# Kernel tuning notes

Measured on AMD Instinct MI355X. Metric: run time of the kernel, lower is better.

## Reference

```python
import jax, jax.numpy as jnp
import numpy as np

NH = 12  # attention heads (bert-base)


def _ln(x, s, b, eps=1e-12):
    mu = x.mean(-1, keepdims=True)
    var = ((x - mu) ** 2).mean(-1, keepdims=True)
    return (x - mu) / jnp.sqrt(var + eps) * s + b


def _forward(input_ids, token_type_ids, attention_mask, word_emb, pos_emb, type_emb,
             emb_ln_s, emb_ln_b, memory, q_w, q_b, k_w, k_b, v_w, v_b, o_w, o_b,
             ln1_s, ln1_b, f_w1, f_b1, f_w2, f_b2, ln2_s, ln2_b,
             key_w1, key_b1, key_w2, key_b2, val_w1, val_b1, val_w2, val_b2):
    B, S = input_ids.shape
    M, H = memory.shape
    T = S + M
    m = attention_mask.astype(jnp.int32)          # [B,S] 0/1
    L = m.sum(-1)                                 # [B] number of real tokens
    tok_emb = word_emb[input_ids]                 # [B,S,H]
    # stable argsort puts mask==1 positions first (in original order), then mask==0
    order = jnp.argsort(1 - m, axis=-1)           # [B,S]
    p = jnp.arange(T)[None, :]                    # [1,T]
    Lb = L[:, None]
    # output layout per sample: [real tokens (L), memory (M), pad tokens (S-L)]
    src_p = jnp.clip(jnp.where(p < Lb, p, p - M), 0, S - 1)
    src_idx = jnp.take_along_axis(order, src_p, axis=1)                  # [B,T]
    gathered = jnp.take_along_axis(tok_emb, src_idx[..., None], axis=1)  # [B,T,H]
    is_mem = (p >= Lb) & (p < Lb + M)
    mem_idx = jnp.clip(p - Lb, 0, M - 1)
    emb = jnp.where(is_mem[..., None], memory[mem_idx], gathered)        # spliced embeds
    att = (p < Lb + M).astype(emb.dtype)                                 # [B,T]
    tt = jnp.where(p < Lb, jnp.take_along_axis(token_type_ids.astype(jnp.int32), src_idx, axis=1), 1)
    # --- BERT encoder on inputs_embeds ---
    x = _ln(emb + pos_emb[None, :T] + type_emb[tt], emb_ln_s, emb_ln_b)
    bias = ((1.0 - att) * -10000.0)[:, None, None, :]                    # [B,1,1,T]
    dh = H // NH
    for l in range(q_w.shape[0]):
        q = (x @ q_w[l] + q_b[l]).reshape(B, T, NH, dh)
        k = (x @ k_w[l] + k_b[l]).reshape(B, T, NH, dh)
        v = (x @ v_w[l] + v_b[l]).reshape(B, T, NH, dh)
        s = jnp.einsum('bqhd,bkhd->bhqk', q, k) / jnp.sqrt(jnp.asarray(dh, x.dtype)) + bias
        a = jax.nn.softmax(s, axis=-1)
        ctx = jnp.einsum('bhqk,bkhd->bqhd', a, v).reshape(B, T, H)
        x = _ln(x + ctx @ o_w[l] + o_b[l], ln1_s[l], ln1_b[l])
        h = jax.nn.gelu(x @ f_w1[l] + f_b1[l], approximate=False)
        x = _ln(x + h @ f_w2[l] + f_b2[l], ln2_s[l], ln2_b[l])
    # --- gated key/value softmax pooling (get_rep_no_vae) ---
    value = jnp.tanh(jax.nn.relu(x @ val_w1 + val_b1) @ val_w2 + val_b2)       # [B,T,E]
    weight = jax.nn.sigmoid(jax.nn.relu(x @ key_w1 + key_b1) @ key_w2 + key_b2)  # [B,T,E]
    pool_mask = jnp.where(tt == 1, -jnp.inf, 0.0).astype(x.dtype)[..., None]   # [B,T,1]
    fw = jax.nn.softmax(weight + pool_mask, axis=-2)  # softmax over token dim
    return jax.nn.relu((fw * value).sum(-2))          # [B,E]


def setup_inputs() -> dict:
    key = jax.random.key(0)
    ks = jax.random.split(key, 20)
    B, S, M, H, E, V, NL, FF = 8, 512, 64, 768, 512, 30522, 2, 3072
    def rn(k, shape, s=0.02):
        return jax.random.normal(k, shape, jnp.float32) * s
    return {
        'input_ids': jax.random.randint(ks[0], (B, S), 0, V),
        'token_type_ids': jnp.zeros((B, S), jnp.int32),
        'attention_mask': jax.random.randint(ks[1], (B, S), 0, 2),
        'word_emb': rn(ks[2], (V, H)),
        'pos_emb': rn(ks[3], (S + M, H)),
        'type_emb': rn(ks[4], (2, H)),
        'emb_ln_s': jnp.ones((H,), jnp.float32), 'emb_ln_b': jnp.zeros((H,), jnp.float32),
        'memory': rn(ks[5], (M, H), 1.0),
        'q_w': rn(ks[6], (NL, H, H)), 'q_b': jnp.zeros((NL, H), jnp.float32),
        'k_w': rn(ks[7], (NL, H, H)), 'k_b': jnp.zeros((NL, H), jnp.float32),
        'v_w': rn(ks[8], (NL, H, H)), 'v_b': jnp.zeros((NL, H), jnp.float32),
        'o_w': rn(ks[9], (NL, H, H)), 'o_b': jnp.zeros((NL, H), jnp.float32),
        'ln1_s': jnp.ones((NL, H), jnp.float32), 'ln1_b': jnp.zeros((NL, H), jnp.float32),
        'f_w1': rn(ks[10], (NL, H, FF)), 'f_b1': jnp.zeros((NL, FF), jnp.float32),
        'f_w2': rn(ks[11], (NL, FF, H)), 'f_b2': jnp.zeros((NL, H), jnp.float32),
        'ln2_s': jnp.ones((NL, H), jnp.float32), 'ln2_b': jnp.zeros((NL, H), jnp.float32),
        'key_w1': rn(ks[12], (H, 2 * H)), 'key_b1': jnp.zeros((2 * H,), jnp.float32),
        'key_w2': rn(ks[13], (2 * H, E)), 'key_b2': jnp.zeros((E,), jnp.float32),
        'val_w1': rn(ks[14], (H, 2 * E)), 'val_b1': jnp.zeros((2 * E,), jnp.float32),
        'val_w2': rn(ks[15], (2 * E, E)), 'val_b2': jnp.zeros((E,), jnp.float32),
    }


def reference(input_ids, token_type_ids, attention_mask, word_emb, pos_emb, type_emb,
              emb_ln_s, emb_ln_b, memory, q_w, q_b, k_w, k_b, v_w, v_b, o_w, o_b,
              ln1_s, ln1_b, f_w1, f_b1, f_w2, f_b2, ln2_s, ln2_b,
              key_w1, key_b1, key_w2, key_b2, val_w1, val_b1, val_w2, val_b2):
    return _forward(input_ids, token_type_ids, attention_mask, word_emb, pos_emb, type_emb,
                    emb_ln_s, emb_ln_b, memory, q_w, q_b, k_w, k_b, v_w, v_b, o_w, o_b,
                    ln1_s, ln1_b, f_w1, f_b1, f_w2, f_b2, ln2_s, ln2_b,
                    key_w1, key_b1, key_w2, key_b2, val_w1, val_b1, val_w2, val_b2)
```

## Files before the change

kernel.cpp:

```cpp
#include <hip/hip_runtime.h>
#include <hip/hip_bf16.h>

#define B 8
#define S 512
#define MM 64
#define T 576
#define H 768
#define NH 12
#define DH 64
#define FF 3072
#define E 512
#define NL 2

typedef __attribute__((ext_vector_type(8))) short bf16x8;
typedef __attribute__((ext_vector_type(4))) float f32x4;

__device__ inline unsigned short bf16_rne(float f) {
    unsigned u = __builtin_bit_cast(unsigned, f);
    unsigned r = u + 0x7FFFu + ((u >> 16) & 1u);
    return (unsigned short)(r >> 16);
}

__device__ inline f32x4 mfma16(bf16x8 a, bf16x8 b, f32x4 c) {
    return __builtin_amdgcn_mfma_f32_16x16x32_bf16(a, b, c, 0, 0, 0);
}

__device__ inline void load_lds16(const void* g, void* l) {
    __builtin_amdgcn_global_load_lds((const __attribute__((address_space(1))) void*)g,
                                     (__attribute__((address_space(3))) void*)l, 16, 0, 0);
}

__global__ void order_kernel(const int* __restrict__ mask, int* __restrict__ ord,
                             int* __restrict__ Larr) {
    __shared__ int ps[S];
    int b = blockIdx.x;
    int t = threadIdx.x;
    int mv = (mask[b * S + t] != 0) ? 1 : 0;
    ps[t] = mv;
    __syncthreads();
    for (int off = 1; off < S; off <<= 1) {
        int v = ps[t];
        int add = (t >= off) ? ps[t - off] : 0;
        __syncthreads();
        ps[t] = v + add;
        __syncthreads();
    }
    int L = ps[S - 1];
    int rank = mv ? (ps[t] - 1) : (L + (t - ps[t]));
    ord[b * S + rank] = t;
    if (t == 0) Larr[b] = L;
}

__global__ void embed_kernel(const int* __restrict__ ids, const int* __restrict__ toktype,
                             const int* __restrict__ ord, const int* __restrict__ Larr,
                             int* __restrict__ boff, int* __restrict__ rowb,
                             const float* __restrict__ word_emb, const float* __restrict__ pos_emb,
                             const float* __restrict__ type_emb, const float* __restrict__ memory,
                             const float* __restrict__ lns, const float* __restrict__ lnb,
                             float* __restrict__ x, unsigned short* __restrict__ xb,
                             int* __restrict__ ttarr) {
    int t = blockIdx.x;
    int b = blockIdx.y;
    int pre[B + 1];
    {
        int acc = 0;
        #pragma unroll
        for (int b2 = 0; b2 < B; ++b2) { pre[b2] = acc; acc += Larr[b2] + MM; }
        pre[B] = acc;
    }
    int Lb = Larr[b];
    int tid = threadIdx.x;
    if (t == 0 && b == 0) {
        if (tid <= B) boff[tid] = pre[tid];
        for (int r = tid; r < B * T; r += 256) {
            int bb = 0;
            #pragma unroll
            for (int b2 = 1; b2 < B; ++b2) bb += (r >= pre[b2]) ? 1 : 0;
            rowb[r] = bb;
        }
    }
    if (t >= Lb + MM) return;
    int row = pre[b] + t;
    int tt;
    const float* src;
    if (t < Lb) {
        int sp = ord[b * S + t];
        tt = toktype[b * S + sp];
        src = &word_emb[(size_t)ids[b * S + sp] * H];
    } else {
        tt = 1;
        src = &memory[(size_t)(t - Lb) * H];
    }
    __shared__ float rowv[H];
    __shared__ float r1[256], r2[256];
    float lsum = 0.f, lsq = 0.f;
    for (int hh = tid; hh < H; hh += 256) {
        float v = src[hh] + pos_emb[(size_t)t * H + hh] + type_emb[(size_t)tt * H + hh];
        rowv[hh] = v;
        lsum += v;
        lsq += v * v;
    }
    r1[tid] = lsum; r2[tid] = lsq;
    __syncthreads();
    for (int s = 128; s > 0; s >>= 1) {
        if (tid < s) { r1[tid] += r1[tid + s]; r2[tid] += r2[tid + s]; }
        __syncthreads();
    }
    float mu = r1[0] / H;
    float var = r2[0] / H - mu * mu;
    float inv = rsqrtf(var + 1e-12f);
    for (int hh = tid; hh < H; hh += 256) {
        float v = (rowv[hh] - mu) * inv * lns[hh] + lnb[hh];
        x[(size_t)row * H + hh] = v;
        xb[(size_t)row * H + hh] = bf16_rne(v);
    }
    if (tid == 0) ttarr[row] = tt;
}

#define ACT_NONE 0
#define ACT_RELU 1
#define ACT_GELU 2
#define ACT_SIGMOID 3
#define ACT_TANH 4

template <int ACT>
__device__ inline float apply_act(float v) {
    if constexpr (ACT == ACT_RELU) return fmaxf(v, 0.f);
    else if constexpr (ACT == ACT_GELU) {
        float y = v * 0.70710678118654752f;
        float a = fabsf(y);
        float t = 1.f / (1.f + 0.3275911f * a);
        float poly = t * (0.254829592f + t * (-0.284496736f + t * (1.421413741f +
                     t * (-1.453152027f + t * 1.061405429f))));
        float e = poly * exp2f(-a * a * 1.4426950408889634f);
        float erfv = 1.f - e;
        erfv = (y < 0.f) ? -erfv : erfv;
        return 0.5f * v * (1.f + erfv);
    }
    else if constexpr (ACT == ACT_SIGMOID) return 1.f / (1.f + expf(-v));
    else if constexpr (ACT == ACT_TANH) return tanhf(v);
    else return v;
}

struct TDesc { const float* src; unsigned dstoff; int Kd; int Nd; int tile0; };
struct TTab { TDesc d[16]; int n; };

__global__ __launch_bounds__(256) void transpose_all(TTab tab, unsigned short* __restrict__ dstbase) {
    int tile = blockIdx.x;
    int mi = 0;
    #pragma unroll
    for (int i = 1; i < 16; ++i)
        if (i < tab.n && tab.d[i].tile0 <= tile) mi = i;
    TDesc d = tab.d[mi];
    int rel = tile - d.tile0;
    int tilesK = d.Kd >> 5;
    int kt = rel % tilesK, nt = rel / tilesK;
    __shared__ float ts[32][33];
    int k0 = kt * 32, n0 = nt * 32;
    int tx = threadIdx.x & 31, ty = threadIdx.x >> 5;
    #pragma unroll
    for (int r = 0; r < 4; ++r) {
        int kk = ty + r * 8;
        ts[kk][tx] = d.src[(size_t)(k0 + kk) * d.Nd + n0 + tx];
    }
    __syncthreads();
    unsigned short* Wt = dstbase + d.dstoff;
    #pragma unroll
    for (int r = 0; r < 4; ++r) {
        int nn = ty + r * 8;
        Wt[(size_t)(n0 + nn) * d.Kd + k0 + tx] = bf16_rne(ts[tx][nn]);
    }
}

#define EPI_F32   0
#define EPI_BF16  1
#define EPI_QKV   2
#define EPI_SPLIT2 3

template <int ACT, int EPI, int NSPLIT>
__global__ __launch_bounds__(256) void mfma_gemm(
    const unsigned short* __restrict__ A, const unsigned short* __restrict__ Bt,
    const float* __restrict__ b0, const float* __restrict__ b1, const float* __restrict__ b2,
    int sp1, int sp2,
    float* __restrict__ Cf, float* __restrict__ Cf2,
    float* __restrict__ Cf3, float* __restrict__ Cf4,
    unsigned short* __restrict__ Cb, unsigned short* __restrict__ Cb2,
    unsigned short* __restrict__ Vt, int n2w,
    const int* __restrict__ boffs, const int* __restrict__ rowb,
    int Mdim, int Ndim, int Kdim) {
    __shared__ unsigned short As[2][128 * 32];
    __shared__ unsigned short Bs[2][128 * 32];

    const int bn = blockIdx.x * 128, bm = blockIdx.y * 128;

    const int Mtot = boffs[B];
    if (bm >= Mtot) return;

    const int z = (NSPLIT > 1) ? blockIdx.z : 0;
    const int Klocal = Kdim / NSPLIT;
    const int koff = z * Klocal;

    const int tid = threadIdx.x;
    const int w = tid >> 6, lane = tid & 63;
    const int lr = lane & 15, g = lane >> 4;
    const int wr = w >> 1, wc = w & 1;
    f32x4 acc[4][4] = {};

    const int srow = w * 32 + (lane >> 2);
    const int kc = (((lane & 3) ^ ((lane >> 4) & 3)) * 8);
    const unsigned short* ga0 = A + (size_t)(bm + srow) * Kdim + kc;
    const unsigned short* ga1 = A + (size_t)(bm + srow + 16) * Kdim + kc;
    const unsigned short* gb0 = Bt + (size_t)(bn + srow) * Kdim + kc;
    const unsigned short* gb1 = Bt + (size_t)(bn + srow + 16) * Kdim + kc;
    const int d0 = (w * 32) * 32, d1 = (w * 32 + 16) * 32;

    const int sw = ((g ^ ((lr >> 2) & 3)) & 3) * 8;

    auto stage = [&](int pp, int k0) {
        load_lds16(ga0 + k0, &As[pp][d0]);
        load_lds16(ga1 + k0, &As[pp][d1]);
        load_lds16(gb0 + k0, &Bs[pp][d0]);
        load_lds16(gb1 + k0, &Bs[pp][d1]);
    };
    auto compute = [&](int pp) {
        bf16x8 af[4], bfr[4];
        #pragma unroll
        for (int i = 0; i < 4; ++i)
            af[i] = *(const bf16x8*)&As[pp][(wr * 64 + i * 16 + lr) * 32 + sw];
        #pragma unroll
        for (int j = 0; j < 4; ++j)
            bfr[j] = *(const bf16x8*)&Bs[pp][(wc * 64 + j * 16 + lr) * 32 + sw];
        __builtin_amdgcn_s_setprio(1);
        #pragma unroll
        for (int i = 0; i < 4; ++i)
            #pragma unroll
            for (int j = 0; j < 4; ++j)
                acc[i][j] = mfma16(af[i], bfr[j], acc[i][j]);
        __builtin_amdgcn_s_setprio(0);
    };

    const int nk = Klocal >> 5;
    stage(0, koff);
    int p = 0;
    for (int s = 0; s < nk; ++s) {
        if (s + 1 < nk) {
            stage(p ^ 1, koff + (s + 1) * 32);
            asm volatile("s_waitcnt vmcnt(4)" ::: "memory");
        } else {
            asm volatile("s_waitcnt vmcnt(0)" ::: "memory");
        }
        __builtin_amdgcn_s_barrier();
        __builtin_amdgcn_sched_barrier(0);
        compute(p);
        __builtin_amdgcn_sched_barrier(0);
        __builtin_amdgcn_s_barrier();
        __builtin_amdgcn_sched_barrier(0);
        p ^= 1;
    }

    float* Cdst = (z == 0) ? Cf : (z == 1) ? Cf2 : (z == 2) ? Cf3 : Cf4;
    #pragma unroll
    for (int i = 0; i < 4; ++i) {
        const int row0 = bm + wr * 64 + i * 16 + 4 * g;
        #pragma unroll
        for (int j = 0; j < 4; ++j) {
            const int col = bn + wc * 64 + j * 16 + lr;
            float bv = (NSPLIT > 1 && z != 0) ? 0.f
                     : ((col < sp1) ? b0[col] : (col < sp2 ? b1[col - sp1] : b2[col - sp2]));
            float vv[4];
            #pragma unroll
            for (int r = 0; r < 4; ++r) vv[r] = apply_act<ACT>(acc[i][j][r] + bv);
            if constexpr (EPI == EPI_F32) {
                #pragma unroll
                for (int r = 0; r < 4; ++r) Cdst[(size_t)(row0 + r) * Ndim + col] = vv[r];
            } else if constexpr (EPI == EPI_BF16) {
                #pragma unroll
                for (int r = 0; r < 4; ++r) Cb[(size_t)(row0 + r) * Ndim + col] = bf16_rne(vv[r]);
            } else if constexpr (EPI == EPI_QKV) {
                if (col < 1536) {
                    #pragma unroll
                    for (int r = 0; r < 4; ++r) Cb[(size_t)(row0 + r) * 1536 + col] = bf16_rne(vv[r]);
                } else {
                    int c2 = col - 1536;
                    int hh2 = c2 >> 6, dd = c2 & 63;
                    int bb = rowb[row0];
                    if (row0 + 3 < Mtot && rowb[row0 + 3] == bb) {
                        int t0 = row0 - boffs[bb];
                        unsigned lo = (unsigned)bf16_rne(vv[0]) | ((unsigned)bf16_rne(vv[1]) << 16);
                        unsigned hi = (unsigned)bf16_rne(vv[2]) | ((unsigned)bf16_rne(vv[3]) << 16);
                        size_t idxv = (((size_t)bb * NH + hh2) * DH + dd) * T + t0;
                        *(uint2*)&Vt[idxv] = make_uint2(lo, hi);
                    } else {
                        #pragma unroll
                        for (int r = 0; r < 4; ++r) {
                            int rr = row0 + r;
                            if (rr < Mtot) {
                                int b2 = rowb[rr];
                                int t2 = rr - boffs[b2];
                                Vt[(((size_t)b2 * NH + hh2) * DH + dd) * T + t2] = bf16_rne(vv[r]);
                            }
                        }
                    }
                }
            } else {
                if (col < sp1) {
                    #pragma unroll
                    for (int r = 0; r < 4; ++r) Cb[(size_t)(row0 + r) * sp1 + col] = bf16_rne(vv[r]);
                } else {
                    #pragma unroll
                    for (int r = 0; r < 4; ++r)
                        Cb2[(size_t)(row0 + r) * n2w + (col - sp1)] = bf16_rne(vv[r]);
                }
            }
        }
    }
}

__global__ __launch_bounds__(256) void head2_gemm(
    const unsigned short* __restrict__ Ak, const unsigned short* __restrict__ Btk,
    const float* __restrict__ biask,
    const unsigned short* __restrict__ Av, const unsigned short* __restrict__ Btv,
    const float* __restrict__ biasv,
    float* __restrict__ P0, float* __restrict__ P1, float* __restrict__ P2, float* __restrict__ P3,
    float* __restrict__ V0, float* __restrict__ V1, float* __restrict__ V2, float* __restrict__ V3,
    const int* __restrict__ boffs) {
    __shared__ unsigned short As[2][128 * 32];
    __shared__ unsigned short Bs[2][128 * 32];

    const int bn = blockIdx.x * 128, bm = blockIdx.y * 128;
    const int Mtot = boffs[B];
    if (bm >= Mtot) return;

    const int z = blockIdx.z;
    const int isval = z >> 2, zk = z & 3;
    const unsigned short* A  = isval ? Av : Ak;
    const unsigned short* Bt = isval ? Btv : Btk;
    const float* bias = isval ? biasv : biask;
    const int Kdim = isval ? 1024 : 1536;
    const int Klocal = Kdim >> 2;
    const int koff = zk * Klocal;
    float* Cdst = isval ? ((zk == 0) ? V0 : (zk == 1) ? V1 : (zk == 2) ? V2 : V3)
                        : ((zk == 0) ? P0 : (zk == 1) ? P1 : (zk == 2) ? P2 : P3);

    const int tid = threadIdx.x;
    const int w = tid >> 6, lane = tid & 63;
    const int lr = lane & 15, g = lane >> 4;
    const int wr = w >> 1, wc = w & 1;
    f32x4 acc[4][4] = {};

    const int srow = w * 32 + (lane >> 2);
    const int kc = (((lane & 3) ^ ((lane >> 4) & 3)) * 8);
    const unsigned short* ga0 = A + (size_t)(bm + srow) * Kdim + kc;
    const unsigned short* ga1 = A + (size_t)(bm + srow + 16) * Kdim + kc;
    const unsigned short* gb0 = Bt + (size_t)(bn + srow) * Kdim + kc;
    const unsigned short* gb1 = Bt + (size_t)(bn + srow + 16) * Kdim + kc;
    const int d0 = (w * 32) * 32, d1 = (w * 32 + 16) * 32;
    const int sw = ((g ^ ((lr >> 2) & 3)) & 3) * 8;

    auto stage = [&](int pp, int k0) {
        load_lds16(ga0 + k0, &As[pp][d0]);
        load_lds16(ga1 + k0, &As[pp][d1]);
        load_lds16(gb0 + k0, &Bs[pp][d0]);
        load_lds16(gb1 + k0, &Bs[pp][d1]);
    };
    auto compute = [&](int pp) {
        bf16x8 af[4], bfr[4];
        #pragma unroll
        for (int i = 0; i < 4; ++i)
            af[i] = *(const bf16x8*)&As[pp][(wr * 64 + i * 16 + lr) * 32 + sw];
        #pragma unroll
        for (int j = 0; j < 4; ++j)
            bfr[j] = *(const bf16x8*)&Bs[pp][(wc * 64 + j * 16 + lr) * 32 + sw];
        __builtin_amdgcn_s_setprio(1);
        #pragma unroll
        for (int i = 0; i < 4; ++i)
            #pragma unroll
            for (int j = 0; j < 4; ++j)
                acc[i][j] = mfma16(af[i], bfr[j], acc[i][j]);
        __builtin_amdgcn_s_setprio(0);
    };

    const int nk = Klocal >> 5;
    stage(0, koff);
    int p = 0;
    for (int s = 0; s < nk; ++s) {
        if (s + 1 < nk) {
            stage(p ^ 1, koff + (s + 1) * 32);
            asm volatile("s_waitcnt vmcnt(4)" ::: "memory");
        } else {
            asm volatile("s_waitcnt vmcnt(0)" ::: "memory");
        }
        __builtin_amdgcn_s_barrier();
        __builtin_amdgcn_sched_barrier(0);
        compute(p);
        __builtin_amdgcn_sched_barrier(0);
        __builtin_amdgcn_s_barrier();
        __builtin_amdgcn_sched_barrier(0);
        p ^= 1;
    }

    #pragma unroll
    for (int i = 0; i < 4; ++i) {
        const int row0 = bm + wr * 64 + i * 16 + 4 * g;
        #pragma unroll
        for (int j = 0; j < 4; ++j) {
            const int col = bn + wc * 64 + j * 16 + lr;
            float bv = (zk == 0) ? bias[col] : 0.f;
            #pragma unroll
            for (int r = 0; r < 4; ++r)
                Cdst[(size_t)(row0 + r) * E + col] = acc[i][j][r] + bv;
        }
    }
}

#define C2 0.180336880111116670f
#define MB2 14426.950408889634f

__global__ __launch_bounds__(256) void attn_mfma(
    const unsigned short* __restrict__ QK, const unsigned short* __restrict__ Vt,
    const int* __restrict__ Larr, const int* __restrict__ boffs,
    unsigned short* __restrict__ ctxb) {
    const int n = blockIdx.x;
    const int xcd = n & 7, k = n >> 3;
    const int p = xcd * 12 + k / 9, qt = k % 9;
    const int b = p / NH, h = p % NH;
    const int LbMM = Larr[b] + MM;
    if (qt * 64 >= LbMM) return;
    const int w = threadIdx.x >> 6, lane = threadIdx.x & 63;
    const int q0 = qt * 64 + w * 16;
    if (q0 >= LbMM) return;
    const int base = boffs[b];
    const int lr = lane & 15, g = lane >> 4;
    __shared__ unsigned short P[4][16][72];
    const unsigned short* qrow = QK + (size_t)(base + q0 + lr) * 1536 + h * 64;
    bf16x8 qf0 = *(const bf16x8*)(qrow + 8 * g);
    bf16x8 qf1 = *(const bf16x8*)(qrow + 32 + 8 * g);
    f32x4 ctx[4] = {};
    float m_run = -1e30f, l_run = 0.f;
    const size_t vbase = ((size_t)b * NH + h) * DH;
    for (int kt = 0; kt < LbMM; kt += 64) {
        f32x4 sf[4];
        #pragma unroll
        for (int i = 0; i < 4; ++i) {
            const unsigned short* krow =
                QK + (size_t)(base + kt + 16 * i + lr) * 1536 + 768 + h * 64;
            bf16x8 kf0 = *(const bf16x8*)(krow + 8 * g);
            bf16x8 kf1 = *(const bf16x8*)(krow + 32 + 8 * g);
            f32x4 s = {};
            s = mfma16(kf0, qf0, s);
            s = mfma16(kf1, qf1, s);
            sf[i] = s;
        }
        float tmax = -1e30f;
        #pragma unroll
        for (int i = 0; i < 4; ++i)
            #pragma unroll
            for (int r = 0; r < 4; ++r) {
                int key = kt + 16 * i + 4 * g + r;
                float v = sf[i][r] * C2 + (key < LbMM ? 0.f : -MB2);
                sf[i][r] = v;
                tmax = fmaxf(tmax, v);
            }
        tmax = fmaxf(tmax, __shfl_xor(tmax, 16));
        tmax = fmaxf(tmax, __shfl_xor(tmax, 32));
        float m_new = fmaxf(m_run, tmax);
        float scale = exp2f(m_run - m_new);
        m_run = m_new;
        float psum = 0.f;
        #pragma unroll
        for (int i = 0; i < 4; ++i)
            #pragma unroll
            for (int r = 0; r < 4; ++r) {
                float pv = exp2f(sf[i][r] - m_new);
                sf[i][r] = pv;
                psum += pv;
            }
        l_run = l_run * scale + psum;
        float f0 = __shfl(scale, 4 * g + 0);
        float f1 = __shfl(scale, 4 * g + 1);
        float f2 = __shfl(scale, 4 * g + 2);
        float f3 = __shfl(scale, 4 * g + 3);
        #pragma unroll
        for (int j = 0; j < 4; ++j) {
            ctx[j][0] *= f0; ctx[j][1] *= f1; ctx[j][2] *= f2; ctx[j][3] *= f3;
        }
        #pragma unroll
        for (int i = 0; i < 4; ++i) {
            unsigned lo = (unsigned)bf16_rne(sf[i][0]) | ((unsigned)bf16_rne(sf[i][1]) << 16);
            unsigned hi = (unsigned)bf16_rne(sf[i][2]) | ((unsigned)bf16_rne(sf[i][3]) << 16);
            *(unsigned*)&P[w][lr][16 * i + 4 * g] = lo;
            *(unsigned*)&P[w][lr][16 * i + 4 * g + 2] = hi;
        }
        asm volatile("s_waitcnt lgkmcnt(0)" ::: "memory");
        __builtin_amdgcn_sched_barrier(0);
        #pragma unroll
        for (int s2 = 0; s2 < 2; ++s2) {
            bf16x8 pa = *(const bf16x8*)&P[w][lr][32 * s2 + 8 * g];
            #pragma unroll
            for (int j = 0; j < 4; ++j) {
                const unsigned short* vrow =
                    Vt + (vbase + 16 * j + lr) * T + kt + 32 * s2 + 8 * g;
                bf16x8 vf = *(const bf16x8*)vrow;
                ctx[j] = mfma16(pa, vf, ctx[j]);
            }
        }
        asm volatile("s_waitcnt lgkmcnt(0)" ::: "memory");
        __builtin_amdgcn_sched_barrier(0);
    }
    l_run += __shfl_xor(l_run, 16);
    l_run += __shfl_xor(l_run, 32);
    float inv = 1.f / l_run;
    float i0 = __shfl(inv, 4 * g + 0);
    float i1 = __shfl(inv, 4 * g + 1);
    float i2 = __shfl(inv, 4 * g + 2);
    float i3 = __shfl(inv, 4 * g + 3);
    float sc[4] = {i0, i1, i2, i3};
    #pragma unroll
    for (int j = 0; j < 4; ++j)
        #pragma unroll
        for (int r = 0; r < 4; ++r) {
            int rl = q0 + 4 * g + r;
            if (rl < LbMM)
                ctxb[(size_t)(base + rl) * H + h * 64 + 16 * j + lr] =
                    bf16_rne(ctx[j][r] * sc[r]);
        }
}

__global__ void lnres_kernel(float* __restrict__ x, const float* __restrict__ d1,
                             const float* __restrict__ d2, const float* __restrict__ d3,
                             const float* __restrict__ d4,
                             const float* __restrict__ s, const float* __restrict__ bvec,
                             unsigned short* __restrict__ xb, const int* __restrict__ mtotp) {
    int r = blockIdx.x;
    if (r >= mtotp[0]) return;
    int tid = threadIdx.x;
    __shared__ float4 row[H / 4];
    __shared__ float r1[256], r2[256];
    float lsum = 0.f, lsq = 0.f;
    size_t off4 = (size_t)r * (H / 4);
    if (tid < H / 4) {
        float4 a = ((const float4*)x)[off4 + tid];
        float4 p1 = ((const float4*)d1)[off4 + tid];
        float4 p2 = ((const float4*)d2)[off4 + tid];
        float4 p3 = ((const float4*)d3)[off4 + tid];
        float4 p4 = ((const float4*)d4)[off4 + tid];
        float4 v = make_float4(a.x + p1.x + p2.x + p3.x + p4.x,
                               a.y + p1.y + p2.y + p3.y + p4.y,
                               a.z + p1.z + p2.z + p3.z + p4.z,
                               a.w + p1.w + p2.w + p3.w + p4.w);
        row[tid] = v;
        lsum = v.x + v.y + v.z + v.w;
        lsq = v.x * v.x + v.y * v.y + v.z * v.z + v.w * v.w;
    }
    r1[tid] = lsum; r2[tid] = lsq;
    __syncthreads();
    for (int ss = 128; ss > 0; ss >>= 1) {
        if (tid < ss) { r1[tid] += r1[tid + ss]; r2[tid] += r2[tid + ss]; }
        __syncthreads();
    }
    float mu = r1[0] / H;
    float var = r2[0] / H - mu * mu;
    float inv = rsqrtf(var + 1e-12f);
    if (tid < H / 4) {
        float4 v = row[tid];
        const float4 sv = ((const float4*)s)[tid];
        const float4 bv = ((const float4*)bvec)[tid];
        float4 o = make_float4((v.x - mu) * inv * sv.x + bv.x,
                               (v.y - mu) * inv * sv.y + bv.y,
                               (v.z - mu) * inv * sv.z + bv.z,
                               (v.w - mu) * inv * sv.w + bv.w);
        ((float4*)x)[off4 + tid] = o;
        ushort4 ob = make_ushort4(bf16_rne(o.x), bf16_rne(o.y), bf16_rne(o.z), bf16_rne(o.w));
        *(ushort4*)&xb[(size_t)r * H + tid * 4] = ob;
    }
}

__global__ __launch_bounds__(256) void pool_kernel(
    const float* __restrict__ w0, const float* __restrict__ w1,
    const float* __restrict__ w2, const float* __restrict__ w3,
    const float* __restrict__ v0, const float* __restrict__ v1,
    const float* __restrict__ v2, const float* __restrict__ v3,
    const int* __restrict__ ttarr, const int* __restrict__ boffs,
    float* __restrict__ out) {
    int b = blockIdx.x;
    int le = threadIdx.x & 31;
    int e = blockIdx.y * 32 + le;
    int tg = threadIdx.x >> 5;
    int base = boffs[b];
    int nrow = boffs[b + 1] - base;
    __shared__ int ttl[T];
    __shared__ float red[8][33];
    for (int t = threadIdx.x; t < nrow; t += 256) ttl[t] = ttarr[base + t];
    __syncthreads();
    float mx = -1e30f;
    for (int t = tg; t < nrow; t += 8) {
        if (ttl[t] == 1) continue;
        size_t idx = (size_t)(base + t) * E + e;
        float w = 1.f / (1.f + expf(-(w0[idx] + w1[idx] + w2[idx] + w3[idx])));
        mx = fmaxf(mx, w);
    }
    red[tg][le] = mx;
    __syncthreads();
    #pragma unroll
    for (int i = 0; i < 8; ++i) mx = fmaxf(mx, red[i][le]);
    float den = 0.f, num = 0.f;
    for (int t = tg; t < nrow; t += 8) {
        if (ttl[t] == 1) continue;
        size_t idx = (size_t)(base + t) * E + e;
        float w = 1.f / (1.f + expf(-(w0[idx] + w1[idx] + w2[idx] + w3[idx])));
        float vval = tanhf(v0[idx] + v1[idx] + v2[idx] + v3[idx]);
        float ew = expf(w - mx);
        den += ew;
        num = fmaf(ew, vval, num);
    }
    __syncthreads();
    red[tg][le] = den;
    __syncthreads();
    float dtot = 0.f;
    #pragma unroll
    for (int i = 0; i < 8; ++i) dtot += red[i][le];
    __syncthreads();
    red[tg][le] = num;
    __syncthreads();
    float ntot = 0.f;
    #pragma unroll
    for (int i = 0; i < 8; ++i) ntot += red[i][le];
    if (tg == 0) out[(size_t)b * E + e] = fmaxf(ntot / dtot, 0.f);
}

extern "C" void kernel_launch(void* const* d_in, const int* in_sizes, int n_in,
                              void* d_out, int out_size, void* d_ws, size_t ws_size,
                              hipStream_t stream) {
    const int*   input_ids  = (const int*)d_in[0];
    const int*   token_type = (const int*)d_in[1];
    const int*   attn_mask  = (const int*)d_in[2];
    const float* word_emb   = (const float*)d_in[3];
    const float* pos_emb    = (const float*)d_in[4];
    const float* type_emb   = (const float*)d_in[5];
    const float* emb_ln_s   = (const float*)d_in[6];
    const float* emb_ln_b   = (const float*)d_in[7];
    const float* memory     = (const float*)d_in[8];
    const float* q_w  = (const float*)d_in[9];
    const float* q_b  = (const float*)d_in[10];
    const float* k_w  = (const float*)d_in[11];
    const float* k_b  = (const float*)d_in[12];
    const float* v_w  = (const float*)d_in[13];
    const float* v_b  = (const float*)d_in[14];
    const float* o_w  = (const float*)d_in[15];
    const float* o_b  = (const float*)d_in[16];
    const float* ln1_s = (const float*)d_in[17];
    const float* ln1_b = (const float*)d_in[18];
    const float* f_w1  = (const float*)d_in[19];
    const float* f_b1  = (const float*)d_in[20];
    const float* f_w2  = (const float*)d_in[21];
    const float* f_b2  = (const float*)d_in[22];
    const float* ln2_s = (const float*)d_in[23];
    const float* ln2_b = (const float*)d_in[24];
    const float* key_w1 = (const float*)d_in[25];
    const float* key_b1 = (const float*)d_in[26];
    const float* key_w2 = (const float*)d_in[27];
    const float* key_b2 = (const float*)d_in[28];
    const float* val_w1 = (const float*)d_in[29];
    const float* val_b1 = (const float*)d_in[30];
    const float* val_w2 = (const float*)d_in[31];
    const float* val_b2 = (const float*)d_in[32];
    float* out = (float*)d_out;

    char* ws = (char*)d_ws;
    size_t off = 0;
    auto alloc = [&](size_t bytes) {
        void* p = ws + off;
        off += (bytes + 255) & ~(size_t)255;
        return p;
    };
    const size_t BT  = (size_t)B * T;
    const size_t BTH = BT * H;

    int*   ord   = (int*)alloc((size_t)B * S * 4);
    int*   Larr  = (int*)alloc(64);
    int*   boff  = (int*)alloc((B + 1) * 4);
    int*   rowb  = (int*)alloc(BT * 4);
    int*   ttarr = (int*)alloc(BT * 4);
    float* x     = (float*)alloc(BTH * 4);
    unsigned short* xb   = (unsigned short*)alloc(BTH * 2);
    unsigned short* reg1 = (unsigned short*)alloc(BT * FF * 2);
    float* P0 = (float*)alloc(BTH * 4);
    float* P1 = (float*)alloc(BTH * 4);
    float* P2 = (float*)alloc(BTH * 4);
    float* P3 = (float*)alloc(BTH * 4);
    float* V0 = (float*)alloc(BT * E * 4);
    float* V1 = (float*)alloc(BT * E * 4);
    float* V2 = (float*)alloc(BT * E * 4);
    float* V3 = (float*)alloc(BT * E * 4);
    unsigned short* wt = (unsigned short*)alloc((size_t)17432576 * 2);

    unsigned short* qkb  = reg1;
    unsigned short* Vtb  = reg1 + BT * 1536;
    unsigned short* ctxb = reg1 + BT * 1536 + BTH;
    unsigned short* hb   = reg1;
    unsigned short* key1b = reg1;
    unsigned short* val1b = reg1 + BT * 1536;

    unsigned short* wt_head = wt + (size_t)14155776;
    unsigned short* wt_kv1 = wt_head;
    unsigned short* wt_k2 = wt_head + (size_t)2560 * 768;
    unsigned short* wt_v2 = wt_k2 + (size_t)512 * 1536;

    const int Mrows = (int)BT;
    const size_t HH = (size_t)H * H;
    const int BIG = 1 << 30;
    const int* mtotp = boff + B;

    hipLaunchKernelGGL(order_kernel, dim3(B), dim3(S), 0, stream, attn_mask, ord, Larr);

    {
        TTab tab;
        tab.n = 16;
        for (int l = 0; l < NL; ++l) {
            unsigned base = (unsigned)(l * 7077888);
            int t0 = l * 6912;
            tab.d[l * 6 + 0] = { q_w + l * HH,              base,                        H,  H,  t0        };
            tab.d[l * 6 + 1] = { k_w + l * HH,              base + 768u * 768u,          H,  H,  t0 + 576  };
            tab.d[l * 6 + 2] = { v_w + l * HH,              base + 1536u * 768u,         H,  H,  t0 + 1152 };
            tab.d[l * 6 + 3] = { o_w + l * HH,              base + 2304u * 768u,         H,  H,  t0 + 1728 };
            tab.d[l * 6 + 4] = { f_w1 + (size_t)l * H * FF, base + 3072u * 768u,         H,  FF, t0 + 2304 };
            tab.d[l * 6 + 5] = { f_w2 + (size_t)l * FF * H, base + 6144u * 768u,         FF, H,  t0 + 4608 };
        }
        tab.d[12] = { key_w1, 14155776u,                    H,     2 * H, 13824 };
        tab.d[13] = { val_w1, 14155776u + 1536u * 768u,     H,     2 * E, 14976 };
        tab.d[14] = { key_w2, 16121856u,                    2 * H, E,     15744 };
        tab.d[15] = { val_w2, 16908288u,                    2 * E, E,     16512 };
        hipLaunchKernelGGL(transpose_all, dim3(17024), dim3(256), 0, stream, tab, wt);
    }

    hipLaunchKernelGGL(embed_kernel, dim3(T, B), dim3(256), 0, stream,
                       input_ids, token_type, ord, Larr, boff, rowb,
                       word_emb, pos_emb, type_emb,
                       memory, emb_ln_s, emb_ln_b, x, xb, ttarr);

    for (int l = 0; l < NL; ++l) {
        unsigned short* wt_l   = wt + (size_t)l * 7077888;
        unsigned short* wt_qkv = wt_l;
        unsigned short* wt_o   = wt_l + (size_t)2304 * 768;
        unsigned short* wt_f1  = wt_o + (size_t)768 * 768;
        unsigned short* wt_f2  = wt_f1 + (size_t)3072 * 768;

        mfma_gemm<ACT_NONE, EPI_QKV, 1><<<dim3(18, 36), 256, 0, stream>>>(
            xb, wt_qkv, q_b + (size_t)l * H, k_b + (size_t)l * H, v_b + (size_t)l * H,
            768, 1536, nullptr, nullptr, nullptr, nullptr, qkb, nullptr, Vtb, 0,
            boff, rowb, Mrows, 2304, H);
        hipLaunchKernelGGL(attn_mfma, dim3(864), dim3(256), 0, stream,
                           qkb, Vtb, Larr, boff, ctxb);
        mfma_gemm<ACT_NONE, EPI_F32, 4><<<dim3(6, 36, 4), 256, 0, stream>>>(
            ctxb, wt_o, o_b + (size_t)l * H, nullptr, nullptr, BIG, BIG,
            P0, P1, P2, P3, nullptr, nullptr, nullptr, 0, boff, rowb, Mrows, H, H);
        hipLaunchKernelGGL(lnres_kernel, dim3((int)BT), dim3(256), 0, stream,
                           x, P0, P1, P2, P3, ln1_s + (size_t)l * H, ln1_b + (size_t)l * H,
                           xb, mtotp);
        mfma_gemm<ACT_GELU, EPI_BF16, 1><<<dim3(24, 36), 256, 0, stream>>>(
            xb, wt_f1, f_b1 + (size_t)l * FF, nullptr, nullptr, BIG, BIG,
            nullptr, nullptr, nullptr, nullptr, hb, nullptr, nullptr, 0,
            boff, rowb, Mrows, FF, H);
        mfma_gemm<ACT_NONE, EPI_F32, 4><<<dim3(6, 36, 4), 256, 0, stream>>>(
            hb, wt_f2, f_b2 + (size_t)l * H, nullptr, nullptr, BIG, BIG,
            P0, P1, P2, P3, nullptr, nullptr, nullptr, 0, boff, rowb, Mrows, H, FF);
        hipLaunchKernelGGL(lnres_kernel, dim3((int)BT), dim3(256), 0, stream,
                           x, P0, P1, P2, P3, ln2_s + (size_t)l * H, ln2_b + (size_t)l * H,
                           xb, mtotp);
    }

    mfma_gemm<ACT_RELU, EPI_SPLIT2, 1><<<dim3(20, 36), 256, 0, stream>>>(
        xb, wt_kv1, key_b1, val_b1, nullptr, 1536, BIG,
        nullptr, nullptr, nullptr, nullptr, key1b, val1b, nullptr, 1024,
        boff, rowb, Mrows, 2560, H);
    head2_gemm<<<dim3(4, 36, 8), 256, 0, stream>>>(
        key1b, wt_k2, key_b2, val1b, wt_v2, val_b2,
        P0, P1, P2, P3, V0, V1, V2, V3, boff);
    hipLaunchKernelGGL(pool_kernel, dim3(B, E / 32), dim3(256), 0, stream,
                       P0, P1, P2, P3, V0, V1, V2, V3, ttarr, boff, out);
}
```

Before: 463.5 us.

## Triple-buffer GEMM LDS stages to drop trailing barrier; fuse order scan into transpose

The two MFMA GEMM kernels move from double to triple LDS buffering, so the second barrier per k-step can be removed. The next stage now writes into a buffer other than the one still being read. The mask prefix-scan order kernel is folded into the weight transpose launch as extra blocks, which saves one kernel launch. Triple buffering raises LDS use per block from 32KB to 48KB, which may reduce occupancy. Removing the barrier is only safe if no wave can get more than one stage ahead, which depends on the remaining barrier.

```diff
diff --git a/kernel.cpp b/kernel.cpp
--- a/kernel.cpp
+++ b/kernel.cpp
@@ -28,27 +28,6 @@
 __device__ inline void load_lds16(const void* g, void* l) {
     __builtin_amdgcn_global_load_lds((const __attribute__((address_space(1))) void*)g,
                                      (__attribute__((address_space(3))) void*)l, 16, 0, 0);
-}
-
-__global__ void order_kernel(const int* __restrict__ mask, int* __restrict__ ord,
-                             int* __restrict__ Larr) {
-    __shared__ int ps[S];
-    int b = blockIdx.x;
-    int t = threadIdx.x;
-    int mv = (mask[b * S + t] != 0) ? 1 : 0;
-    ps[t] = mv;
-    __syncthreads();
-    for (int off = 1; off < S; off <<= 1) {
-        int v = ps[t];
-        int add = (t >= off) ? ps[t - off] : 0;
-        __syncthreads();
-        ps[t] = v + add;
-        __syncthreads();
-    }
-    int L = ps[S - 1];
-    int rank = mv ? (ps[t] - 1) : (L + (t - ps[t]));
-    ord[b * S + rank] = t;
-    if (t == 0) Larr[b] = L;
 }
 
 __global__ void embed_kernel(const int* __restrict__ ids, const int* __restrict__ toktype,
@@ -142,11 +121,37 @@
     else return v;
 }
 
+#define NT_TILES 17024
 struct TDesc { const float* src; unsigned dstoff; int Kd; int Nd; int tile0; };
 struct TTab { TDesc d[16]; int n; };
 
-__global__ __launch_bounds__(256) void transpose_all(TTab tab, unsigned short* __restrict__ dstbase) {
+__global__ __launch_bounds__(256) void transpose_all(TTab tab, unsigned short* __restrict__ dstbase,
+                                                     const int* __restrict__ mask,
+                                                     int* __restrict__ ord, int* __restrict__ Larr) {
     int tile = blockIdx.x;
+    int tid = threadIdx.x;
+    if (tile >= NT_TILES) {
+        int b = tile - NT_TILES;
+        __shared__ int ps[S];
+        int m0 = (mask[b * S + tid] != 0) ? 1 : 0;
+        int m1 = (mask[b * S + tid + 256] != 0) ? 1 : 0;
+        ps[tid] = m0; ps[tid + 256] = m1;
+        __syncthreads();
+        for (int off2 = 1; off2 < S; off2 <<= 1) {
+            int a0 = (tid >= off2) ? ps[tid - off2] : 0;
+            int a1 = (tid + 256 >= off2) ? ps[tid + 256 - off2] : 0;
+            __syncthreads();
+            ps[tid] += a0; ps[tid + 256] += a1;
+            __syncthreads();
+        }
+        int L = ps[S - 1];
+        int r0 = m0 ? (ps[tid] - 1) : (L + (tid - ps[tid]));
+        int r1 = m1 ? (ps[tid + 256] - 1) : (L + (tid + 256 - ps[tid + 256]));
+        ord[b * S + r0] = tid;
+        ord[b * S + r1] = tid + 256;
+        if (tid == 0) Larr[b] = L;
+        return;
+    }
     int mi = 0;
     #pragma unroll
     for (int i = 1; i < 16; ++i)
@@ -157,7 +162,7 @@
     int kt = rel % tilesK, nt = rel / tilesK;
     __shared__ float ts[32][33];
     int k0 = kt * 32, n0 = nt * 32;
-    int tx = threadIdx.x & 31, ty = threadIdx.x >> 5;
+    int tx = tid & 31, ty = tid >> 5;
     #pragma unroll
     for (int r = 0; r < 4; ++r) {
         int kk = ty + r * 8;
@@ -188,8 +193,8 @@
     unsigned short* __restrict__ Vt, int n2w,
     const int* __restrict__ boffs, const int* __restrict__ rowb,
     int Mdim, int Ndim, int Kdim) {
-    __shared__ unsigned short As[2][128 * 32];
-    __shared__ unsigned short Bs[2][128 * 32];
+    __shared__ unsigned short As[3][128 * 32];
+    __shared__ unsigned short Bs[3][128 * 32];
 
     const int bn = blockIdx.x * 128, bm = blockIdx.y * 128;
 
@@ -244,7 +249,8 @@
     int p = 0;
     for (int s = 0; s < nk; ++s) {
         if (s + 1 < nk) {
-            stage(p ^ 1, koff + (s + 1) * 32);
+            int pn = p + 1; if (pn == 3) pn = 0;
+            stage(pn, koff + (s + 1) * 32);
             asm volatile("s_waitcnt vmcnt(4)" ::: "memory");
         } else {
             asm volatile("s_waitcnt vmcnt(0)" ::: "memory");
@@ -253,9 +259,7 @@
         __builtin_amdgcn_sched_barrier(0);
         compute(p);
         __builtin_amdgcn_sched_barrier(0);
-        __builtin_amdgcn_s_barrier();
-        __builtin_amdgcn_sched_barrier(0);
-        p ^= 1;
+        p = (p == 2) ? 0 : p + 1;
     }
 
     float* Cdst = (z == 0) ? Cf : (z == 1) ? Cf2 : (z == 2) ? Cf3 : Cf4;
@@ -324,8 +328,8 @@
     float* __restrict__ P0, float* __restrict__ P1, float* __restrict__ P2, float* __restrict__ P3,
     float* __restrict__ V0, float* __restrict__ V1, float* __restrict__ V2, float* __restrict__ V3,
     const int* __restrict__ boffs) {
-    __shared__ unsigned short As[2][128 * 32];
-    __shared__ unsigned short Bs[2][128 * 32];
+    __shared__ unsigned short As[3][128 * 32];
+    __shared__ unsigned short Bs[3][128 * 32];
 
     const int bn = blockIdx.x * 128, bm = blockIdx.y * 128;
     const int Mtot = boffs[B];
@@ -385,7 +389,8 @@
     int p = 0;
     for (int s = 0; s < nk; ++s) {
         if (s + 1 < nk) {
-            stage(p ^ 1, koff + (s + 1) * 32);
+            int pn = p + 1; if (pn == 3) pn = 0;
+            stage(pn, koff + (s + 1) * 32);
             asm volatile("s_waitcnt vmcnt(4)" ::: "memory");
         } else {
             asm volatile("s_waitcnt vmcnt(0)" ::: "memory");
@@ -394,9 +399,7 @@
         __builtin_amdgcn_sched_barrier(0);
         compute(p);
         __builtin_amdgcn_sched_barrier(0);
-        __builtin_amdgcn_s_barrier();
-        __builtin_amdgcn_sched_barrier(0);
-        p ^= 1;
+        p = (p == 2) ? 0 : p + 1;
     }
 
     #pragma unroll
@@ -711,8 +714,6 @@
     const int BIG = 1 << 30;
     const int* mtotp = boff + B;
 
-    hipLaunchKernelGGL(order_kernel, dim3(B), dim3(S), 0, stream, attn_mask, ord, Larr);
-
     {
         TTab tab;
         tab.n = 16;
@@ -730,7 +731,8 @@
         tab.d[13] = { val_w1, 14155776u + 1536u * 768u,     H,     2 * E, 14976 };
         tab.d[14] = { key_w2, 16121856u,                    2 * H, E,     15744 };
         tab.d[15] = { val_w2, 16908288u,                    2 * E, E,     16512 };
-        hipLaunchKernelGGL(transpose_all, dim3(17024), dim3(256), 0, stream, tab, wt);
+        hipLaunchKernelGGL(transpose_all, dim3(NT_TILES + B), dim3(256), 0, stream,
+                           tab, wt, attn_mask, ord, Larr);
     }
 
     hipLaunchKernelGGL(embed_kernel, dim3(T, B), dim3(256), 0, stream,
```

Result: faster. 451.4 us (median of 2 runs) (-2.6%).
